# Kernel tuning notes

Hardware: AMD Instinct MI355X
Metric: run time of the kernel (lower is better)

The kernel has to match this reference:

```python
import jax, jax.numpy as jnp
import numpy as np

HEADS = 4
DIM_HEAD = 32
CHUNK = 1024
GROUPS = 8
EPS = 1e-5


def setup_inputs() -> dict:
    key = jax.random.key(0)
    k1, k2, k3 = jax.random.split(key, 3)
    b, dim, h, w = 8, 64, 96, 96
    inner = HEADS * DIM_HEAD  # 128
    x = jax.random.normal(k1, (b, dim, h, w), dtype=jnp.float32)
    W_qkv = jax.random.normal(k2, (3 * inner, dim), dtype=jnp.float32) * (1.0 / np.sqrt(dim))
    W_out = jax.random.normal(k3, (dim, inner), dtype=jnp.float32) * (1.0 / np.sqrt(inner))
    b_out = jnp.zeros((dim,), dtype=jnp.float32)
    gamma = jnp.ones((dim,), dtype=jnp.float32)
    beta = jnp.zeros((dim,), dtype=jnp.float32)
    return {"x": x, "W_qkv": W_qkv, "W_out": W_out, "b_out": b_out,
            "gamma": gamma, "beta": beta}


def reference(x, W_qkv, W_out, b_out, gamma, beta):
    b, c, h, w = x.shape
    n = h * w
    nch = n // CHUNK  # number of full chunks (n chosen divisible by CHUNK)
    d = DIM_HEAD
    BH = b * HEADS

    # 1x1 conv (no bias) == matmul over channel dim
    xf = x.reshape(b, c, n)
    qkv = jnp.einsum('oc,bcn->bon', W_qkv, xf)          # [b, 3*inner, n]
    q, k, v = jnp.split(qkv, 3, axis=1)                  # each [b, inner, n]

    def chunkify(t):
        # [b, inner, n] -> [BH, nch, d, CHUNK]; slicing i:i+CHUNK on last axis
        # equals reshaping n -> (nch, CHUNK) in order.
        return t.reshape(BH, d, nch, CHUNK).transpose(0, 2, 1, 3)

    qc, kc, vc = chunkify(q), chunkify(k), chunkify(v)

    qs = jax.nn.softmax(qc, axis=-1)  # softmax over chunk spatial positions
    ks = jax.nn.softmax(kc, axis=-2)  # softmax over head channels

    # context = k_chunk^T @ v_chunk : [BH, nch, CHUNK, CHUNK]
    ctx = jnp.einsum('gkdi,gkdj->gkij', ks, vc)
    # chunk_out = q_chunk @ context : [BH, nch, d, CHUNK]
    out = jnp.einsum('gkdi,gkij->gkdj', qs, ctx)

    # concat chunks back along spatial dim, reshape to image layout
    out = out.transpose(0, 2, 1, 3).reshape(b, HEADS * d, h, w)

    # to_out: 1x1 conv with bias, then GroupNorm(8, dim)
    y = jnp.einsum('oc,bchw->bohw', W_out, out) + b_out[None, :, None, None]

    yg = y.reshape(b, GROUPS, c // GROUPS, h, w)
    mu = jnp.mean(yg, axis=(2, 3, 4), keepdims=True)
    var = jnp.var(yg, axis=(2, 3, 4), keepdims=True)
    yn = ((yg - mu) * jax.lax.rsqrt(var + EPS)).reshape(b, c, h, w)
    return yn * gamma[None, :, None, None] + beta[None, :, None, None]
```

## Files before the change

kernel.cpp:

```cpp
#include <hip/hip_runtime.h>
#include <hip/hip_bf16.h>

#define N_POS 9216
#define NCHUNK 9
#define CHUNKN 1024
#define BATCH 8
#define CDIM 64
#define HEADS 4
#define DHEAD 32
#define INNER 128
#define GROUPS 8
#define EPS 1e-5f

#define QKV_SZ (BATCH*384*N_POS)
#define QKV_BYTES ((size_t)QKV_SZ * 2)
#define P_SZ (BATCH*HEADS*NCHUNK*1024)
#define ZTOT (128 + P_SZ)

typedef __attribute__((ext_vector_type(8))) short short8;
typedef __attribute__((ext_vector_type(4))) float f32x4;

static __device__ inline unsigned pk2(float a, float b) {
    __hip_bfloat162 h2(__float2bfloat16(a), __float2bfloat16(b));
    return *reinterpret_cast<unsigned*>(&h2);
}
static __device__ inline float bf2f(short s) {
    union { unsigned u; float f; } c; c.u = ((unsigned)(unsigned short)s) << 16; return c.f;
}

__global__ __launch_bounds__(256) void zero_kernel(float* __restrict__ p) {
    int i = blockIdx.x * 256 + threadIdx.x;
    if (i < ZTOT) p[i] = 0.f;
}

__global__ __launch_bounds__(256) void qkv_kernel(const float* __restrict__ x,
        const float* __restrict__ Wqkv, __hip_bfloat16* __restrict__ qkv) {
    int n0 = blockIdx.x * 256;
    int m0 = blockIdx.y * 128;
    int b  = blockIdx.z;
    __shared__ __hip_bfloat16 xs[256][72];
    __shared__ __hip_bfloat16 wsm[128][72];
    int t = threadIdx.x;
    int w = t >> 6, l = t & 63;

    {
        const float* xb = x + (size_t)b * CDIM * N_POS + n0 + t;
        #pragma unroll
        for (int c = 0; c < 64; c += 4) {
            float v0 = xb[(size_t)(c + 0) * N_POS];
            float v1 = xb[(size_t)(c + 1) * N_POS];
            float v2 = xb[(size_t)(c + 2) * N_POS];
            float v3 = xb[(size_t)(c + 3) * N_POS];
            uint2 u; u.x = pk2(v0, v1); u.y = pk2(v2, v3);
            *reinterpret_cast<uint2*>(&xs[t][c]) = u;
        }
    }
    {
        int m = t >> 1, ch = (t & 1) * 32;
        const float4* wr = (const float4*)(Wqkv + (size_t)(m0 + m) * CDIM + ch);
        #pragma unroll
        for (int j = 0; j < 8; ++j) {
            float4 v = wr[j];
            uint2 u; u.x = pk2(v.x, v.y); u.y = pk2(v.z, v.w);
            *reinterpret_cast<uint2*>(&wsm[m][ch + j * 4]) = u;
        }
    }
    __syncthreads();

    int lrow = l & 15, lquad = l >> 4;
    f32x4 acc[8][4];
    #pragma unroll
    for (int mt = 0; mt < 8; ++mt)
        #pragma unroll
        for (int nt = 0; nt < 4; ++nt) acc[mt][nt] = (f32x4){0.f, 0.f, 0.f, 0.f};

    #pragma unroll
    for (int ks = 0; ks < 2; ++ks) {
        int k0 = lquad * 8 + ks * 32;
        short8 bfr[4];
        #pragma unroll
        for (int nt = 0; nt < 4; ++nt) {
            int n = w * 64 + nt * 16 + lrow;
            bfr[nt] = *reinterpret_cast<const short8*>(&xs[n][k0]);
        }
        #pragma unroll
        for (int mt = 0; mt < 8; ++mt) {
            short8 afr = *reinterpret_cast<const short8*>(&wsm[mt * 16 + lrow][k0]);
            #pragma unroll
            for (int nt = 0; nt < 4; ++nt)
                acc[mt][nt] = __builtin_amdgcn_mfma_f32_16x16x32_bf16(afr, bfr[nt], acc[mt][nt], 0, 0, 0);
        }
    }

    if (blockIdx.y == 2) {
        __hip_bfloat16* vt = qkv + ((size_t)b * 384 + 256) * N_POS;
        #pragma unroll
        for (int mt = 0; mt < 8; ++mt)
            #pragma unroll
            for (int nt = 0; nt < 4; ++nt) {
                int n = n0 + w * 64 + nt * 16 + lrow;
                uint2 u;
                u.x = pk2(acc[mt][nt][0], acc[mt][nt][1]);
                u.y = pk2(acc[mt][nt][2], acc[mt][nt][3]);
                *reinterpret_cast<uint2*>(vt + (size_t)n * 128 + mt * 16 + lquad * 4) = u;
            }
    } else {
        __hip_bfloat16* outp = qkv + ((size_t)b * 384 + m0) * N_POS + n0;
        #pragma unroll
        for (int mt = 0; mt < 8; ++mt)
            #pragma unroll
            for (int nt = 0; nt < 4; ++nt) {
                int n = w * 64 + nt * 16 + lrow;
                #pragma unroll
                for (int r = 0; r < 4; ++r) {
                    int o = mt * 16 + lquad * 4 + r;
                    outp[(size_t)o * N_POS + n] = __float2bfloat16(acc[mt][nt][r]);
                }
            }
    }
}

__global__ __launch_bounds__(256) void smat_part(const __hip_bfloat16* __restrict__ qkv,
        float* __restrict__ Pg) {
    int bh = blockIdx.x;
    int ck = blockIdx.y;
    int pt = blockIdx.z;
    int b = bh >> 2, h = bh & 3;
    int p0 = ck * CHUNKN + pt * 256;
    __shared__ __hip_bfloat16 qsb[32][264];
    __shared__ __hip_bfloat16 ksb[32][264];
    int t = threadIdx.x, w = t >> 6, l = t & 63;
    const __hip_bfloat16* qbase = qkv + ((size_t)b * 384 + h * 32) * N_POS + p0 + t;
    const __hip_bfloat16* kbase = qkv + ((size_t)b * 384 + 128 + h * 32) * N_POS + p0 + t;
    {
        float kr[32]; float mx = -1e30f;
        #pragma unroll
        for (int d = 0; d < 32; ++d) { kr[d] = bf2f(*(const short*)(kbase + (size_t)d * N_POS)); mx = fmaxf(mx, kr[d]); }
        float s = 0.f;
        #pragma unroll
        for (int d = 0; d < 32; ++d) { kr[d] = __expf(kr[d] - mx); s += kr[d]; }
        float is = 1.f / s;
        #pragma unroll
        for (int d = 0; d < 32; ++d) ksb[d][t] = __float2bfloat16(kr[d] * is);
    }
    #pragma unroll
    for (int d = 0; d < 32; ++d)
        qsb[d][t] = __float2bfloat16(__expf(bf2f(*(const short*)(qbase + (size_t)d * N_POS))));
    __syncthreads();

    int mt = w >> 1, nt = w & 1;
    int l15 = l & 15, quad = l >> 4;
    f32x4 acc = (f32x4){0.f, 0.f, 0.f, 0.f};
    #pragma unroll
    for (int step = 0; step < 8; ++step) {
        int k0 = step * 32 + quad * 8;
        short8 af = *reinterpret_cast<const short8*>(&qsb[mt * 16 + l15][k0]);
        short8 bf = *reinterpret_cast<const short8*>(&ksb[nt * 16 + l15][k0]);
        acc = __builtin_amdgcn_mfma_f32_16x16x32_bf16(af, bf, acc, 0, 0, 0);
    }
    float* Pp = Pg + ((size_t)bh * NCHUNK + ck) * 1024;
    #pragma unroll
    for (int r = 0; r < 4; ++r)
        atomicAdd(&Pp[(mt * 16 + quad * 4 + r) * 32 + nt * 16 + l15], acc[r]);
}

__global__ __launch_bounds__(256) void umat_kernel(const float* __restrict__ Wout,
        const float* __restrict__ Pg, __hip_bfloat16* __restrict__ Ubf) {
    int ck = blockIdx.x, b = blockIdx.y, h = blockIdx.z;
    int bh = b * 4 + h;
    __shared__ float Pl[32][32];
    __shared__ float iZ[32];
    int t = threadIdx.x;
    const float* Pp = Pg + ((size_t)bh * NCHUNK + ck) * 1024;
    ((float4*)Pl)[t] = ((const float4*)Pp)[t];
    __syncthreads();
    if (t < 32) {
        float s = 0.f;
        #pragma unroll
        for (int c = 0; c < 32; ++c) s += Pl[t][c];
        iZ[t] = 1.f / s;
    }
    __syncthreads();
    int o = t & 63, wv = t >> 6;
    float wz[32];
    {
        const float4* wr = (const float4*)(Wout + (size_t)o * 128 + h * 32);
        #pragma unroll
        for (int j = 0; j < 8; ++j) {
            float4 f = wr[j];
            wz[j*4+0] = f.x * iZ[j*4+0]; wz[j*4+1] = f.y * iZ[j*4+1];
            wz[j*4+2] = f.z * iZ[j*4+2]; wz[j*4+3] = f.w * iZ[j*4+3];
        }
    }
    float ua[8];
    #pragma unroll
    for (int j = 0; j < 8; ++j) ua[j] = 0.f;
    for (int d = 0; d < 32; ++d) {
        float wd = wz[d];
        #pragma unroll
        for (int j = 0; j < 8; ++j) ua[j] += wd * Pl[d][wv * 8 + j];
    }
    uint4 up;
    up.x = pk2(ua[0], ua[1]); up.y = pk2(ua[2], ua[3]);
    up.z = pk2(ua[4], ua[5]); up.w = pk2(ua[6], ua[7]);
    __hip_bfloat16* Up = Ubf + ((size_t)(b * NCHUNK + ck) * 64 + o) * 128 + h * 32 + wv * 8;
    *reinterpret_cast<uint4*>(Up) = up;
}

__global__ __launch_bounds__(256) void y_kernel(const __hip_bfloat16* __restrict__ qkv,
        const __hip_bfloat16* __restrict__ Ubf, const float* __restrict__ bout,
        float* __restrict__ y, float* __restrict__ stats) {
    int bx = blockIdx.x;
    int b  = blockIdx.y;
    int ck = bx >> 3;
    __shared__ float gsum[8], gsq[8];
    int t = threadIdx.x, w = t >> 6, l = t & 63;
    int l15 = l & 15, quad = l >> 4;
    if (t < 8) { gsum[t] = 0.f; gsq[t] = 0.f; }
    __syncthreads();
    const __hip_bfloat16* vt = qkv + ((size_t)b * 384 + 256) * N_POS;
    const __hip_bfloat16* Ub = Ubf + (size_t)(b * NCHUNK + ck) * 64 * 128;
    int nbase = bx * 128 + w * 32;
    f32x4 acc[4][2];
    #pragma unroll
    for (int mt = 0; mt < 4; ++mt) { acc[mt][0] = (f32x4){0,0,0,0}; acc[mt][1] = (f32x4){0,0,0,0}; }
    #pragma unroll
    for (int ks = 0; ks < 4; ++ks) {
        int k0 = ks * 32 + quad * 8;
        short8 bf[2];
        #pragma unroll
        for (int nt = 0; nt < 2; ++nt)
            bf[nt] = *reinterpret_cast<const short8*>(vt + (size_t)(nbase + nt * 16 + l15) * 128 + k0);
        #pragma unroll
        for (int mt = 0; mt < 4; ++mt) {
            short8 af = *reinterpret_cast<const short8*>(Ub + (size_t)(mt * 16 + l15) * 128 + k0);
            acc[mt][0] = __builtin_amdgcn_mfma_f32_16x16x32_bf16(af, bf[0], acc[mt][0], 0, 0, 0);
            acc[mt][1] = __builtin_amdgcn_mfma_f32_16x16x32_bf16(af, bf[1], acc[mt][1], 0, 0, 0);
        }
    }
    float gsl[4], gql[4];
    #pragma unroll
    for (int mt = 0; mt < 4; ++mt) { gsl[mt] = 0.f; gql[mt] = 0.f; }
    float* yb = y + (size_t)b * CDIM * N_POS;
    #pragma unroll
    for (int mt = 0; mt < 4; ++mt) {
        float4 bo = *reinterpret_cast<const float4*>(bout + mt * 16 + quad * 4);
        const float* bop = reinterpret_cast<const float*>(&bo);
        #pragma unroll
        for (int nt = 0; nt < 2; ++nt) {
            int n = nbase + nt * 16 + l15;
            #pragma unroll
            for (int r = 0; r < 4; ++r) {
                int o = mt * 16 + quad * 4 + r;
                float val = acc[mt][nt][r] + bop[r];
                yb[(size_t)o * N_POS + n] = val;
                gsl[mt] += val; gql[mt] += val * val;
            }
        }
    }
    #pragma unroll
    for (int off = 16; off >= 1; off >>= 1) {
        #pragma unroll
        for (int mt = 0; mt < 4; ++mt) {
            gsl[mt] += __shfl_xor(gsl[mt], off, 64);
            gql[mt] += __shfl_xor(gql[mt], off, 64);
        }
    }
    if (l == 0 || l == 32) {
        int qh = quad >> 1;
        #pragma unroll
        for (int mt = 0; mt < 4; ++mt) {
            atomicAdd(&gsum[2 * mt + qh], gsl[mt]);
            atomicAdd(&gsq[2 * mt + qh], gql[mt]);
        }
    }
    __syncthreads();
    if (t < 8) {
        atomicAdd(&stats[(b * 8 + t) * 2],     gsum[t]);
        atomicAdd(&stats[(b * 8 + t) * 2 + 1], gsq[t]);
    }
}

__global__ __launch_bounds__(256) void gn_kernel(float* __restrict__ y,
        const float* __restrict__ stats, const float* __restrict__ gamma,
        const float* __restrict__ beta) {
    int i4 = blockIdx.x * 256 + threadIdx.x;
    if (i4 >= (BATCH * CDIM * N_POS) / 4) return;
    int base = i4 * 4;
    int bc = base / N_POS;
    int c = bc & 63, b = bc >> 6;
    int g = c >> 3;
    float s = stats[(b * 8 + g) * 2], q = stats[(b * 8 + g) * 2 + 1];
    const float invN = 1.f / (8.f * N_POS);
    float mean = s * invN;
    float var = q * invN - mean * mean;
    float sc = rsqrtf(var + EPS);
    float ga = gamma[c] * sc;
    float be = beta[c] - mean * sc * gamma[c];
    float4 v = ((float4*)y)[i4];
    v.x = v.x * ga + be; v.y = v.y * ga + be; v.z = v.z * ga + be; v.w = v.w * ga + be;
    ((float4*)y)[i4] = v;
}

extern "C" void kernel_launch(void* const* d_in, const int* in_sizes, int n_in,
                              void* d_out, int out_size, void* d_ws, size_t ws_size,
                              hipStream_t stream) {
    const float* x     = (const float*)d_in[0];
    const float* Wqkv  = (const float*)d_in[1];
    const float* Wout  = (const float*)d_in[2];
    const float* bout  = (const float*)d_in[3];
    const float* gamma = (const float*)d_in[4];
    const float* beta  = (const float*)d_in[5];
    float* out = (float*)d_out;

    __hip_bfloat16* qkv = (__hip_bfloat16*)d_ws;
    float* stats = (float*)((char*)d_ws + QKV_BYTES);
    float* Pg    = stats + 128;
    __hip_bfloat16* Ubf = (__hip_bfloat16*)(Pg + P_SZ);

    zero_kernel<<<dim3((ZTOT + 255) / 256), 256, 0, stream>>>(stats);
    qkv_kernel<<<dim3(36, 3, BATCH), 256, 0, stream>>>(x, Wqkv, qkv);
    smat_part<<<dim3(32, NCHUNK, 4), 256, 0, stream>>>(qkv, Pg);
    umat_kernel<<<dim3(NCHUNK, BATCH, HEADS), 256, 0, stream>>>(Wout, Pg, Ubf);
    y_kernel<<<dim3(72, BATCH), 256, 0, stream>>>(qkv, Ubf, bout, out, stats);
    gn_kernel<<<dim3((BATCH * CDIM * N_POS / 4 + 255) / 256), 256, 0, stream>>>(out, stats, gamma, beta);
}
```

Baseline: 140.6 us.

## Store Q/K/V position-major via LDS staging and replace atomics with partial buffers

The qkv kernel now writes all three sections (Q, K, V) in position-major [b][n][128] layout. It stages each tile through LDS so the global stores are coalesced 16-byte writes, replacing the strided scalar bf16 stores used for Q and K. smat_part reads Q/K as vectorized 16-byte loads per position, and writes its partial P tiles to four separate buffers instead of using atomicAdd. umat sums the four partials and zeroes the GroupNorm stats, so the separate zero kernel launch is removed. The cost is extra LDS traffic and syncs in qkv and a larger workspace for the partial P buffers.

```diff
diff --git a/kernel.cpp b/kernel.cpp
--- a/kernel.cpp
+++ b/kernel.cpp
@@ -7,15 +7,12 @@
 #define BATCH 8
 #define CDIM 64
 #define HEADS 4
-#define DHEAD 32
-#define INNER 128
 #define GROUPS 8
 #define EPS 1e-5f
 
-#define QKV_SZ (BATCH*384*N_POS)
-#define QKV_BYTES ((size_t)QKV_SZ * 2)
-#define P_SZ (BATCH*HEADS*NCHUNK*1024)
-#define ZTOT (128 + P_SZ)
+#define SEC_SZ ((size_t)BATCH * N_POS * 128)
+#define QKV_BYTES (3 * SEC_SZ * 2)
+#define PPART_SZ ((size_t)32 * NCHUNK * 1024)
 
 typedef __attribute__((ext_vector_type(8))) short short8;
 typedef __attribute__((ext_vector_type(4))) float f32x4;
@@ -28,18 +25,15 @@
     union { unsigned u; float f; } c; c.u = ((unsigned)(unsigned short)s) << 16; return c.f;
 }
 
-__global__ __launch_bounds__(256) void zero_kernel(float* __restrict__ p) {
-    int i = blockIdx.x * 256 + threadIdx.x;
-    if (i < ZTOT) p[i] = 0.f;
-}
-
 __global__ __launch_bounds__(256) void qkv_kernel(const float* __restrict__ x,
         const float* __restrict__ Wqkv, __hip_bfloat16* __restrict__ qkv) {
-    int n0 = blockIdx.x * 256;
-    int m0 = blockIdx.y * 128;
-    int b  = blockIdx.z;
-    __shared__ __hip_bfloat16 xs[256][72];
-    __shared__ __hip_bfloat16 wsm[128][72];
+    int n0  = blockIdx.x * 256;
+    int sec = blockIdx.y;
+    int b   = blockIdx.z;
+    __shared__ __align__(16) char lds_raw[256 * 136 * 2];
+    __hip_bfloat16 (*xs)[72]    = (__hip_bfloat16(*)[72])lds_raw;
+    __hip_bfloat16 (*wsm)[72]   = (__hip_bfloat16(*)[72])(lds_raw + 256*72*2);
+    __hip_bfloat16 (*vbuf)[136] = (__hip_bfloat16(*)[136])lds_raw;
     int t = threadIdx.x;
     int w = t >> 6, l = t & 63;
 
@@ -57,7 +51,7 @@
     }
     {
         int m = t >> 1, ch = (t & 1) * 32;
-        const float4* wr = (const float4*)(Wqkv + (size_t)(m0 + m) * CDIM + ch);
+        const float4* wr = (const float4*)(Wqkv + ((size_t)sec * 128 + m) * CDIM + ch);
         #pragma unroll
         for (int j = 0; j < 8; ++j) {
             float4 v = wr[j];
@@ -91,51 +85,49 @@
                 acc[mt][nt] = __builtin_amdgcn_mfma_f32_16x16x32_bf16(afr, bfr[nt], acc[mt][nt], 0, 0, 0);
         }
     }
-
-    if (blockIdx.y == 2) {
-        __hip_bfloat16* vt = qkv + ((size_t)b * 384 + 256) * N_POS;
-        #pragma unroll
-        for (int mt = 0; mt < 8; ++mt)
-            #pragma unroll
-            for (int nt = 0; nt < 4; ++nt) {
-                int n = n0 + w * 64 + nt * 16 + lrow;
-                uint2 u;
-                u.x = pk2(acc[mt][nt][0], acc[mt][nt][1]);
-                u.y = pk2(acc[mt][nt][2], acc[mt][nt][3]);
-                *reinterpret_cast<uint2*>(vt + (size_t)n * 128 + mt * 16 + lquad * 4) = u;
-            }
-    } else {
-        __hip_bfloat16* outp = qkv + ((size_t)b * 384 + m0) * N_POS + n0;
-        #pragma unroll
-        for (int mt = 0; mt < 8; ++mt)
-            #pragma unroll
-            for (int nt = 0; nt < 4; ++nt) {
-                int n = w * 64 + nt * 16 + lrow;
-                #pragma unroll
-                for (int r = 0; r < 4; ++r) {
-                    int o = mt * 16 + lquad * 4 + r;
-                    outp[(size_t)o * N_POS + n] = __float2bfloat16(acc[mt][nt][r]);
-                }
-            }
+    __syncthreads();
+
+    #pragma unroll
+    for (int mt = 0; mt < 8; ++mt)
+        #pragma unroll
+        for (int nt = 0; nt < 4; ++nt) {
+            int n = w * 64 + nt * 16 + lrow;
+            uint2 u;
+            u.x = pk2(acc[mt][nt][0], acc[mt][nt][1]);
+            u.y = pk2(acc[mt][nt][2], acc[mt][nt][3]);
+            *reinterpret_cast<uint2*>(&vbuf[n][mt * 16 + lquad * 4]) = u;
+        }
+    __syncthreads();
+
+    __hip_bfloat16* outb = qkv + (size_t)sec * SEC_SZ + ((size_t)b * N_POS + n0) * 128;
+    int rg = t >> 4, c0 = (t & 15) * 8;
+    #pragma unroll
+    for (int j = 0; j < 16; ++j) {
+        int r = j * 16 + rg;
+        *reinterpret_cast<uint4*>(outb + (size_t)r * 128 + c0) =
+            *reinterpret_cast<const uint4*>(&vbuf[r][c0]);
     }
 }
 
 __global__ __launch_bounds__(256) void smat_part(const __hip_bfloat16* __restrict__ qkv,
-        float* __restrict__ Pg) {
-    int bh = blockIdx.x;
-    int ck = blockIdx.y;
-    int pt = blockIdx.z;
+        float* __restrict__ Pparts) {
+    int bh = blockIdx.x, ck = blockIdx.y, pt = blockIdx.z;
     int b = bh >> 2, h = bh & 3;
-    int p0 = ck * CHUNKN + pt * 256;
+    int p = ck * CHUNKN + pt * 256 + threadIdx.x;
     __shared__ __hip_bfloat16 qsb[32][264];
     __shared__ __hip_bfloat16 ksb[32][264];
     int t = threadIdx.x, w = t >> 6, l = t & 63;
-    const __hip_bfloat16* qbase = qkv + ((size_t)b * 384 + h * 32) * N_POS + p0 + t;
-    const __hip_bfloat16* kbase = qkv + ((size_t)b * 384 + 128 + h * 32) * N_POS + p0 + t;
-    {
+    const __hip_bfloat16* qp = qkv + ((size_t)b * N_POS + p) * 128 + h * 32;
+    const __hip_bfloat16* kp = qkv + SEC_SZ + ((size_t)b * N_POS + p) * 128 + h * 32;
+    {
+        short8 kv4[4];
+        #pragma unroll
+        for (int j = 0; j < 4; ++j) kv4[j] = *reinterpret_cast<const short8*>(kp + j * 8);
         float kr[32]; float mx = -1e30f;
         #pragma unroll
-        for (int d = 0; d < 32; ++d) { kr[d] = bf2f(*(const short*)(kbase + (size_t)d * N_POS)); mx = fmaxf(mx, kr[d]); }
+        for (int j = 0; j < 4; ++j)
+            #pragma unroll
+            for (int e = 0; e < 8; ++e) { kr[j*8+e] = bf2f(kv4[j][e]); mx = fmaxf(mx, kr[j*8+e]); }
         float s = 0.f;
         #pragma unroll
         for (int d = 0; d < 32; ++d) { kr[d] = __expf(kr[d] - mx); s += kr[d]; }
@@ -143,9 +135,16 @@
         #pragma unroll
         for (int d = 0; d < 32; ++d) ksb[d][t] = __float2bfloat16(kr[d] * is);
     }
-    #pragma unroll
-    for (int d = 0; d < 32; ++d)
-        qsb[d][t] = __float2bfloat16(__expf(bf2f(*(const short*)(qbase + (size_t)d * N_POS))));
+    {
+        short8 qv4[4];
+        #pragma unroll
+        for (int j = 0; j < 4; ++j) qv4[j] = *reinterpret_cast<const short8*>(qp + j * 8);
+        #pragma unroll
+        for (int j = 0; j < 4; ++j)
+            #pragma unroll
+            for (int e = 0; e < 8; ++e)
+                qsb[j*8+e][t] = __float2bfloat16(__expf(bf2f(qv4[j][e])));
+    }
     __syncthreads();
 
     int mt = w >> 1, nt = w & 1;
@@ -158,21 +157,32 @@
         short8 bf = *reinterpret_cast<const short8*>(&ksb[nt * 16 + l15][k0]);
         acc = __builtin_amdgcn_mfma_f32_16x16x32_bf16(af, bf, acc, 0, 0, 0);
     }
-    float* Pp = Pg + ((size_t)bh * NCHUNK + ck) * 1024;
+    float* Pp = Pparts + (size_t)pt * PPART_SZ + ((size_t)bh * NCHUNK + ck) * 1024;
     #pragma unroll
     for (int r = 0; r < 4; ++r)
-        atomicAdd(&Pp[(mt * 16 + quad * 4 + r) * 32 + nt * 16 + l15], acc[r]);
+        Pp[(mt * 16 + quad * 4 + r) * 32 + nt * 16 + l15] = acc[r];
 }
 
 __global__ __launch_bounds__(256) void umat_kernel(const float* __restrict__ Wout,
-        const float* __restrict__ Pg, __hip_bfloat16* __restrict__ Ubf) {
+        const float* __restrict__ Pparts, __hip_bfloat16* __restrict__ Ubf,
+        float* __restrict__ stats) {
     int ck = blockIdx.x, b = blockIdx.y, h = blockIdx.z;
     int bh = b * 4 + h;
+    int t = threadIdx.x;
+    if (ck == 0 && h == 0 && t < 16) stats[b * 16 + t] = 0.f;
     __shared__ float Pl[32][32];
     __shared__ float iZ[32];
-    int t = threadIdx.x;
-    const float* Pp = Pg + ((size_t)bh * NCHUNK + ck) * 1024;
-    ((float4*)Pl)[t] = ((const float4*)Pp)[t];
+    size_t base4 = (((size_t)bh * NCHUNK + ck) * 1024) / 4;
+    {
+        const float4* P0 = (const float4*)Pparts + base4;
+        const float4* P1 = (const float4*)(Pparts + PPART_SZ) + base4;
+        const float4* P2 = (const float4*)(Pparts + 2 * PPART_SZ) + base4;
+        const float4* P3 = (const float4*)(Pparts + 3 * PPART_SZ) + base4;
+        float4 a = P0[t], bb = P1[t], c = P2[t], d = P3[t];
+        float4 s; s.x = a.x+bb.x+c.x+d.x; s.y = a.y+bb.y+c.y+d.y;
+        s.z = a.z+bb.z+c.z+d.z; s.w = a.w+bb.w+c.w+d.w;
+        ((float4*)Pl)[t] = s;
+    }
     __syncthreads();
     if (t < 32) {
         float s = 0.f;
@@ -218,7 +228,7 @@
     int l15 = l & 15, quad = l >> 4;
     if (t < 8) { gsum[t] = 0.f; gsq[t] = 0.f; }
     __syncthreads();
-    const __hip_bfloat16* vt = qkv + ((size_t)b * 384 + 256) * N_POS;
+    const __hip_bfloat16* vt = qkv + 2 * SEC_SZ + (size_t)b * N_POS * 128;
     const __hip_bfloat16* Ub = Ubf + (size_t)(b * NCHUNK + ck) * 64 * 128;
     int nbase = bx * 128 + w * 32;
     f32x4 acc[4][2];
@@ -314,14 +324,13 @@
     float* out = (float*)d_out;
 
     __hip_bfloat16* qkv = (__hip_bfloat16*)d_ws;
-    float* stats = (float*)((char*)d_ws + QKV_BYTES);
-    float* Pg    = stats + 128;
-    __hip_bfloat16* Ubf = (__hip_bfloat16*)(Pg + P_SZ);
-
-    zero_kernel<<<dim3((ZTOT + 255) / 256), 256, 0, stream>>>(stats);
+    float* stats  = (float*)((char*)d_ws + QKV_BYTES);
+    float* Pparts = stats + 128;
+    __hip_bfloat16* Ubf = (__hip_bfloat16*)(Pparts + 4 * PPART_SZ);
+
     qkv_kernel<<<dim3(36, 3, BATCH), 256, 0, stream>>>(x, Wqkv, qkv);
-    smat_part<<<dim3(32, NCHUNK, 4), 256, 0, stream>>>(qkv, Pg);
-    umat_kernel<<<dim3(NCHUNK, BATCH, HEADS), 256, 0, stream>>>(Wout, Pg, Ubf);
+    smat_part<<<dim3(32, NCHUNK, 4), 256, 0, stream>>>(qkv, Pparts);
+    umat_kernel<<<dim3(NCHUNK, BATCH, HEADS), 256, 0, stream>>>(Wout, Pparts, Ubf, stats);
     y_kernel<<<dim3(72, BATCH), 256, 0, stream>>>(qkv, Ubf, bout, out, stats);
     gn_kernel<<<dim3((BATCH * CDIM * N_POS / 4 + 255) / 256), 256, 0, stream>>>(out, stats, gamma, beta);
 }
```

Measured after the change: 133.2 us. 5.2% less time.
